# Kernel tuning notes

Measured on AMD Instinct MI355X. Metric: run time of the kernel, lower is better.

Reference implementation:

```python
import jax, jax.numpy as jnp
import numpy as np

N, M = 8192, 8192
N_POS, N_NEG = 2_000_000, 8_000_000


def setup_inputs() -> dict:
    key = jax.random.key(0)
    k1, k2, k3, k4, k5, k6, k7 = jax.random.split(key, 7)
    return {
        "drug_protein_reconstruct": jax.random.normal(k1, (N, M), dtype=jnp.float32),
        "drug_protein": jax.random.uniform(k2, (N, M), dtype=jnp.float32),
        "alpha": jax.random.uniform(k3, (1,), dtype=jnp.float32),
        "pos_x_index": jax.random.randint(k4, (N_POS,), 0, N, dtype=jnp.int64 if jax.config.jax_enable_x64 else jnp.int32),
        "pos_y_index": jax.random.randint(k5, (N_POS,), 0, M, dtype=jnp.int64 if jax.config.jax_enable_x64 else jnp.int32),
        "neg_x_index": jax.random.randint(k6, (N_NEG,), 0, N, dtype=jnp.int64 if jax.config.jax_enable_x64 else jnp.int32),
        "neg_y_index": jax.random.randint(k7, (N_NEG,), 0, M, dtype=jnp.int64 if jax.config.jax_enable_x64 else jnp.int32),
    }


def reference(drug_protein_reconstruct, drug_protein, alpha,
              pos_x_index, pos_y_index, neg_x_index, neg_y_index):
    # Fused gather -> subtract -> square -> sum (equivalent to dense MSE matrix
    # followed by fancy indexing, but without materializing the full loss_mat).
    a = alpha[0]
    pos_diff = (drug_protein_reconstruct[pos_x_index, pos_y_index]
                - drug_protein[pos_x_index, pos_y_index])
    neg_diff = (drug_protein_reconstruct[neg_x_index, neg_y_index]
                - drug_protein[neg_x_index, neg_y_index])
    pos_sum = jnp.sum(pos_diff * pos_diff)
    neg_sum = jnp.sum(neg_diff * neg_diff)
    return pos_sum * ((1.0 - a) * 0.5) + neg_sum * (a * 0.5)
```

## Files before the change

### kernel.cpp

```cpp
#include <hip/hip_runtime.h>

#define BLOCK 256
#define GRID  2048
#define NBUCK 256
#define PIPT  16
#define PCHUNK (BLOCK * PIPT)

typedef int v4i __attribute__((ext_vector_type(4)));

__device__ __forceinline__ void block_reduce_out(float pos_acc, float neg_acc,
                                                 const float* alpha, float* out) {
    const float a = alpha[0];
    float v = pos_acc * ((1.0f - a) * 0.5f) + neg_acc * (a * 0.5f);
    #pragma unroll
    for (int off = 32; off > 0; off >>= 1)
        v += __shfl_down(v, off, 64);
    __shared__ float sdata[BLOCK / 64];
    const int lane = threadIdx.x & 63;
    const int wave = threadIdx.x >> 6;
    if (lane == 0) sdata[wave] = v;
    __syncthreads();
    if (threadIdx.x == 0) {
        float s = 0.0f;
        #pragma unroll
        for (int w = 0; w < BLOCK / 64; ++w) s += sdata[w];
        if (s != 0.0f) atomicAdd(out, s);
    }
}

__global__ __launch_bounds__(BLOCK) void partition_kernel(
    const int* __restrict__ px, const int* __restrict__ py, int npos,
    const int* __restrict__ nx, const int* __restrict__ ny, int nneg,
    unsigned* __restrict__ items, unsigned* __restrict__ gcnt, int cap,
    const float* __restrict__ R, const float* __restrict__ D,
    const float* __restrict__ alpha, float* __restrict__ out)
{
    __shared__ unsigned s_cnt[NBUCK];
    __shared__ unsigned s_base[NBUCK];
    __shared__ unsigned s_cur[NBUCK];

    const int tid   = threadIdx.x;
    const int total = npos + nneg;
    const int nchunks = (total + PCHUNK - 1) / PCHUNK;

    float pos_acc = 0.0f, neg_acc = 0.0f;

    for (int c = blockIdx.x; c < nchunks; c += gridDim.x) {
        const int run = c * PCHUNK + tid * PIPT;
        const int nval = min(PIPT, max(0, total - run));

        unsigned it[PIPT];
        if (nval == PIPT && run + PIPT <= npos) {
            const v4i* x4 = (const v4i*)(px + run);
            const v4i* y4 = (const v4i*)(py + run);
            #pragma unroll
            for (int q = 0; q < PIPT / 4; ++q) {
                v4i xs = x4[q], ys = y4[q];
                it[q*4+0] = ((unsigned)xs.x << 13) | (unsigned)ys.x;
                it[q*4+1] = ((unsigned)xs.y << 13) | (unsigned)ys.y;
                it[q*4+2] = ((unsigned)xs.z << 13) | (unsigned)ys.z;
                it[q*4+3] = ((unsigned)xs.w << 13) | (unsigned)ys.w;
            }
        } else if (nval == PIPT && run >= npos && (((run - npos) & 3) == 0)) {
            const int j = run - npos;
            const v4i* x4 = (const v4i*)(nx + j);
            const v4i* y4 = (const v4i*)(ny + j);
            #pragma unroll
            for (int q = 0; q < PIPT / 4; ++q) {
                v4i xs = x4[q], ys = y4[q];
                it[q*4+0] = (((unsigned)xs.x << 13) | (unsigned)ys.x) | (1u << 26);
                it[q*4+1] = (((unsigned)xs.y << 13) | (unsigned)ys.y) | (1u << 26);
                it[q*4+2] = (((unsigned)xs.z << 13) | (unsigned)ys.z) | (1u << 26);
                it[q*4+3] = (((unsigned)xs.w << 13) | (unsigned)ys.w) | (1u << 26);
            }
        } else {
            for (int k = 0; k < PIPT; ++k) {
                const int gi = run + k;
                if (k < nval) {
                    if (gi < npos) it[k] = ((unsigned)px[gi] << 13) | (unsigned)py[gi];
                    else {
                        const int j = gi - npos;
                        it[k] = (((unsigned)nx[j] << 13) | (unsigned)ny[j]) | (1u << 26);
                    }
                } else it[k] = 0;
            }
        }

        s_cnt[tid] = 0;
        __syncthreads();
        #pragma unroll
        for (int k = 0; k < PIPT; ++k)
            if (k < nval) atomicAdd(&s_cnt[(it[k] >> 18) & 0xFF], 1u);
        __syncthreads();

        const unsigned cnt = s_cnt[tid];
        if (cnt) s_base[tid] = atomicAdd(&gcnt[tid], cnt);
        s_cur[tid] = 0;
        __syncthreads();

        #pragma unroll
        for (int k = 0; k < PIPT; ++k) {
            if (k < nval) {
                const unsigned b = (it[k] >> 18) & 0xFF;
                const unsigned p = atomicAdd(&s_cur[b], 1u);
                const unsigned gpos = s_base[b] + p;
                if (gpos < (unsigned)cap) {
                    items[(size_t)b * cap + gpos] = it[k];
                } else {
                    const unsigned o = it[k] & 0x3FFFFFFu;
                    const float d = R[o] - D[o];
                    if (it[k] >> 26) neg_acc += d * d; else pos_acc += d * d;
                }
            }
        }
        __syncthreads();
    }

    block_reduce_out(pos_acc, neg_acc, alpha, out);
}

__global__ __launch_bounds__(BLOCK) void gather_kernel(
    const float* __restrict__ R, const float* __restrict__ D,
    const float* __restrict__ alpha,
    const unsigned* __restrict__ items, const unsigned* __restrict__ gcnt,
    int cap, float* __restrict__ out)
{
    const int xcd = blockIdx.x & 7;
    const int g   = blockIdx.x >> 3;
    const unsigned team_stride = (GRID / 8) * BLOCK;

    float pos_acc = 0.0f, neg_acc = 0.0f;

    for (int bi = 0; bi < NBUCK / 8; ++bi) {
        const int b = bi * 8 + xcd;
        const unsigned n = min(gcnt[b], (unsigned)cap);
        const unsigned* ib = items + (size_t)b * cap;
        for (unsigned i = (unsigned)g * BLOCK + threadIdx.x; i < n; i += team_stride) {
            const unsigned it = ib[i];
            const unsigned o = it & 0x3FFFFFFu;
            const float d = R[o] - D[o];
            if (it >> 26) neg_acc += d * d; else pos_acc += d * d;
        }
    }

    block_reduce_out(pos_acc, neg_acc, alpha, out);
}

__global__ __launch_bounds__(BLOCK) void dti_direct_kernel(
    const float* __restrict__ R, const float* __restrict__ D,
    const float* __restrict__ alpha,
    const int* __restrict__ px, const int* __restrict__ py, int npos,
    const int* __restrict__ nx, const int* __restrict__ ny, int nneg,
    float* __restrict__ out)
{
    const int tid = blockIdx.x * BLOCK + threadIdx.x;
    const int stride = gridDim.x * BLOCK;
    float pos_acc = 0.0f, neg_acc = 0.0f;
    {
        const int n4 = npos >> 2;
        const v4i* px4 = (const v4i*)px;
        const v4i* py4 = (const v4i*)py;
        for (int i = tid; i < n4; i += stride) {
            v4i xs = px4[i], ys = py4[i];
            int o0 = (xs.x << 13) + ys.x, o1 = (xs.y << 13) + ys.y;
            int o2 = (xs.z << 13) + ys.z, o3 = (xs.w << 13) + ys.w;
            float d0 = R[o0]-D[o0], d1 = R[o1]-D[o1], d2 = R[o2]-D[o2], d3 = R[o3]-D[o3];
            pos_acc += d0*d0 + d1*d1 + d2*d2 + d3*d3;
        }
        for (int i = (n4 << 2) + tid; i < npos; i += stride) {
            int o = (px[i] << 13) + py[i];
            float d = R[o] - D[o];
            pos_acc += d * d;
        }
    }
    {
        const int n4 = nneg >> 2;
        const v4i* nx4 = (const v4i*)nx;
        const v4i* ny4 = (const v4i*)ny;
        for (int i = tid; i < n4; i += stride) {
            v4i xs = nx4[i], ys = ny4[i];
            int o0 = (xs.x << 13) + ys.x, o1 = (xs.y << 13) + ys.y;
            int o2 = (xs.z << 13) + ys.z, o3 = (xs.w << 13) + ys.w;
            float d0 = R[o0]-D[o0], d1 = R[o1]-D[o1], d2 = R[o2]-D[o2], d3 = R[o3]-D[o3];
            neg_acc += d0*d0 + d1*d1 + d2*d2 + d3*d3;
        }
        for (int i = (n4 << 2) + tid; i < nneg; i += stride) {
            int o = (nx[i] << 13) + ny[i];
            float d = R[o] - D[o];
            neg_acc += d * d;
        }
    }
    block_reduce_out(pos_acc, neg_acc, alpha, out);
}

extern "C" void kernel_launch(void* const* d_in, const int* in_sizes, int n_in,
                              void* d_out, int out_size, void* d_ws, size_t ws_size,
                              hipStream_t stream) {
    const float* R     = (const float*)d_in[0];
    const float* D     = (const float*)d_in[1];
    const float* alpha = (const float*)d_in[2];
    const int*   px    = (const int*)d_in[3];
    const int*   py    = (const int*)d_in[4];
    const int*   nx    = (const int*)d_in[5];
    const int*   ny    = (const int*)d_in[6];
    const int    npos  = in_sizes[3];
    const int    nneg  = in_sizes[5];
    const int    total = npos + nneg;

    float* out = (float*)d_out;
    hipMemsetAsync(out, 0, sizeof(float), stream);

    const int cap = total / NBUCK + total / (NBUCK * 4) + 1024;
    const size_t need = (size_t)NBUCK * cap * sizeof(unsigned) + NBUCK * sizeof(unsigned);

    if (d_ws != nullptr && ws_size >= need) {
        unsigned* items = (unsigned*)d_ws;
        unsigned* gcnt  = items + (size_t)NBUCK * cap;
        hipMemsetAsync(gcnt, 0, NBUCK * sizeof(unsigned), stream);
        partition_kernel<<<GRID, BLOCK, 0, stream>>>(
            px, py, npos, nx, ny, nneg, items, gcnt, cap, R, D, alpha, out);
        gather_kernel<<<GRID, BLOCK, 0, stream>>>(
            R, D, alpha, items, gcnt, cap, out);
    } else {
        dti_direct_kernel<<<GRID, BLOCK, 0, stream>>>(
            R, D, alpha, px, py, npos, nx, ny, nneg, out);
    }
}
```

Baseline: 708.1 us.

## Replace bucketed gather with dense per-element count histogram and streaming loss pass

Adds a path that scatters atomic increments into a byte-per-element count map, using 4-bit positive and 4-bit negative counts packed four elements per word. A second kernel then streams R and D as 16-byte vectors and weights each squared difference by its counts. This swaps random 4-byte gathers and the bucket partition for a mostly sequential sweep of both matrices. The cost is a 64MB memset, scattered global atomics and reading most of R and D. The 4-bit counters can overflow if one element is indexed more than 15 times.

```diff
diff --git a/kernel.cpp b/kernel.cpp
--- a/kernel.cpp
+++ b/kernel.cpp
@@ -6,7 +6,8 @@
 #define PIPT  16
 #define PCHUNK (BLOCK * PIPT)
 
-typedef int v4i __attribute__((ext_vector_type(4)));
+typedef int   v4i __attribute__((ext_vector_type(4)));
+typedef float v4f __attribute__((ext_vector_type(4)));
 
 __device__ __forceinline__ void block_reduce_out(float pos_acc, float neg_acc,
                                                  const float* alpha, float* out) {
@@ -28,6 +29,87 @@
     }
 }
 
+__global__ __launch_bounds__(BLOCK) void count_scatter_kernel(
+    const int* __restrict__ px, const int* __restrict__ py, int npos,
+    const int* __restrict__ nx, const int* __restrict__ ny, int nneg,
+    unsigned* __restrict__ cnt)
+{
+    const int tid    = blockIdx.x * BLOCK + threadIdx.x;
+    const int stride = GRID * BLOCK;
+
+    {
+        const int n4 = npos >> 2;
+        const v4i* x4 = (const v4i*)px;
+        const v4i* y4 = (const v4i*)py;
+        for (int i = tid; i < n4; i += stride) {
+            v4i xs = __builtin_nontemporal_load(&x4[i]);
+            v4i ys = __builtin_nontemporal_load(&y4[i]);
+            unsigned o0 = ((unsigned)xs.x << 13) + (unsigned)ys.x;
+            unsigned o1 = ((unsigned)xs.y << 13) + (unsigned)ys.y;
+            unsigned o2 = ((unsigned)xs.z << 13) + (unsigned)ys.z;
+            unsigned o3 = ((unsigned)xs.w << 13) + (unsigned)ys.w;
+            atomicAdd(&cnt[o0 >> 2], 1u << ((o0 & 3u) * 8u));
+            atomicAdd(&cnt[o1 >> 2], 1u << ((o1 & 3u) * 8u));
+            atomicAdd(&cnt[o2 >> 2], 1u << ((o2 & 3u) * 8u));
+            atomicAdd(&cnt[o3 >> 2], 1u << ((o3 & 3u) * 8u));
+        }
+        for (int i = (n4 << 2) + tid; i < npos; i += stride) {
+            unsigned o = ((unsigned)px[i] << 13) + (unsigned)py[i];
+            atomicAdd(&cnt[o >> 2], 1u << ((o & 3u) * 8u));
+        }
+    }
+    {
+        const int n4 = nneg >> 2;
+        const v4i* x4 = (const v4i*)nx;
+        const v4i* y4 = (const v4i*)ny;
+        for (int i = tid; i < n4; i += stride) {
+            v4i xs = __builtin_nontemporal_load(&x4[i]);
+            v4i ys = __builtin_nontemporal_load(&y4[i]);
+            unsigned o0 = ((unsigned)xs.x << 13) + (unsigned)ys.x;
+            unsigned o1 = ((unsigned)xs.y << 13) + (unsigned)ys.y;
+            unsigned o2 = ((unsigned)xs.z << 13) + (unsigned)ys.z;
+            unsigned o3 = ((unsigned)xs.w << 13) + (unsigned)ys.w;
+            atomicAdd(&cnt[o0 >> 2], 16u << ((o0 & 3u) * 8u));
+            atomicAdd(&cnt[o1 >> 2], 16u << ((o1 & 3u) * 8u));
+            atomicAdd(&cnt[o2 >> 2], 16u << ((o2 & 3u) * 8u));
+            atomicAdd(&cnt[o3 >> 2], 16u << ((o3 & 3u) * 8u));
+        }
+        for (int i = (n4 << 2) + tid; i < nneg; i += stride) {
+            unsigned o = ((unsigned)nx[i] << 13) + (unsigned)ny[i];
+            atomicAdd(&cnt[o >> 2], 16u << ((o & 3u) * 8u));
+        }
+    }
+}
+
+__global__ __launch_bounds__(BLOCK) void dense_loss_kernel(
+    const float* __restrict__ R, const float* __restrict__ D,
+    const float* __restrict__ alpha, const unsigned* __restrict__ cnt,
+    int nwords, float* __restrict__ out)
+{
+    const int tid    = blockIdx.x * BLOCK + threadIdx.x;
+    const int stride = GRID * BLOCK;
+    float pos_acc = 0.0f, neg_acc = 0.0f;
+
+    const v4f* R4 = (const v4f*)R;
+    const v4f* D4 = (const v4f*)D;
+    for (int w = tid; w < nwords; w += stride) {
+        const unsigned c = __builtin_nontemporal_load(&cnt[w]);
+        if (c) {
+            v4f r = __builtin_nontemporal_load(&R4[w]);
+            v4f d = __builtin_nontemporal_load(&D4[w]);
+            #pragma unroll
+            for (int j = 0; j < 4; ++j) {
+                const unsigned b = (c >> (j * 8)) & 0xFFu;
+                const float df = r[j] - d[j];
+                const float d2 = df * df;
+                pos_acc += d2 * (float)(b & 0xFu);
+                neg_acc += d2 * (float)(b >> 4);
+            }
+        }
+    }
+    block_reduce_out(pos_acc, neg_acc, alpha, out);
+}
+
 __global__ __launch_bounds__(BLOCK) void partition_kernel(
     const int* __restrict__ px, const int* __restrict__ py, int npos,
     const int* __restrict__ nx, const int* __restrict__ ny, int nneg,
@@ -93,8 +175,8 @@
             if (k < nval) atomicAdd(&s_cnt[(it[k] >> 18) & 0xFF], 1u);
         __syncthreads();
 
-        const unsigned cnt = s_cnt[tid];
-        if (cnt) s_base[tid] = atomicAdd(&gcnt[tid], cnt);
+        const unsigned cntv = s_cnt[tid];
+        if (cntv) s_base[tid] = atomicAdd(&gcnt[tid], cntv);
         s_cur[tid] = 0;
         __syncthreads();
 
@@ -205,15 +287,27 @@
     const int*   ny    = (const int*)d_in[6];
     const int    npos  = in_sizes[3];
     const int    nneg  = in_sizes[5];
+    const int    nelem = in_sizes[0];
     const int    total = npos + nneg;
 
     float* out = (float*)d_out;
     hipMemsetAsync(out, 0, sizeof(float), stream);
 
+    const size_t need_dense = (size_t)nelem;
+
+    if (d_ws != nullptr && ws_size >= need_dense) {
+        unsigned* cnt = (unsigned*)d_ws;
+        hipMemsetAsync(cnt, 0, need_dense, stream);
+        count_scatter_kernel<<<GRID, BLOCK, 0, stream>>>(
+            px, py, npos, nx, ny, nneg, cnt);
+        dense_loss_kernel<<<GRID, BLOCK, 0, stream>>>(
+            R, D, alpha, cnt, nelem >> 2, out);
+        return;
+    }
+
     const int cap = total / NBUCK + total / (NBUCK * 4) + 1024;
-    const size_t need = (size_t)NBUCK * cap * sizeof(unsigned) + NBUCK * sizeof(unsigned);
-
-    if (d_ws != nullptr && ws_size >= need) {
+    const size_t need_bucket = (size_t)NBUCK * cap * sizeof(unsigned) + NBUCK * sizeof(unsigned);
+    if (d_ws != nullptr && ws_size >= need_bucket) {
         unsigned* items = (unsigned*)d_ws;
         unsigned* gcnt  = items + (size_t)NBUCK * cap;
         hipMemsetAsync(gcnt, 0, NBUCK * sizeof(unsigned), stream);
@@ -221,8 +315,9 @@
             px, py, npos, nx, ny, nneg, items, gcnt, cap, R, D, alpha, out);
         gather_kernel<<<GRID, BLOCK, 0, stream>>>(
             R, D, alpha, items, gcnt, cap, out);
-    } else {
-        dti_direct_kernel<<<GRID, BLOCK, 0, stream>>>(
-            R, D, alpha, px, py, npos, nx, ny, nneg, out);
-    }
-}
+        return;
+    }
+
+    dti_direct_kernel<<<GRID, BLOCK, 0, stream>>>(
+        R, D, alpha, px, py, npos, nx, ny, nneg, out);
+}
```

Result: slower. 909.3 us (+28.4%).

## Stage partitioned items in LDS via block prefix scan for coalesced bucket stores

Applied to the files above, without the earlier changes.

The partition kernel now computes an exclusive prefix scan of per-bucket counts and scatters each chunk's items into a shared-memory buffer sorted by bucket. It then writes them out with consecutive threads handling consecutive slots, so global stores to each bucket become contiguous runs instead of scattered per-thread writes. Index loads and item stores use nontemporal hints, and cap is rounded to a multiple of 4. This adds 16KB of LDS per block and an extra barrier and pass, which may reduce occupancy.

```diff
diff --git a/kernel.cpp b/kernel.cpp
--- a/kernel.cpp
+++ b/kernel.cpp
@@ -36,8 +36,10 @@
     const float* __restrict__ alpha, float* __restrict__ out)
 {
     __shared__ unsigned s_cnt[NBUCK];
-    __shared__ unsigned s_base[NBUCK];
-    __shared__ unsigned s_cur[NBUCK];
+    __shared__ unsigned s_pos[NBUCK];
+    __shared__ unsigned s_gmo[NBUCK];
+    __shared__ unsigned s_wsum[BLOCK/64];
+    __shared__ unsigned s_items[PCHUNK];
 
     const int tid   = threadIdx.x;
     const int total = npos + nneg;
@@ -45,8 +47,8 @@
 
     float pos_acc = 0.0f, neg_acc = 0.0f;
 
-    for (int c = blockIdx.x; c < nchunks; c += gridDim.x) {
-        const int run = c * PCHUNK + tid * PIPT;
+    for (int c = blockIdx.x; c < nchunks; c += GRID) {
+        const int run  = c * PCHUNK + tid * PIPT;
         const int nval = min(PIPT, max(0, total - run));
 
         unsigned it[PIPT];
@@ -55,7 +57,8 @@
             const v4i* y4 = (const v4i*)(py + run);
             #pragma unroll
             for (int q = 0; q < PIPT / 4; ++q) {
-                v4i xs = x4[q], ys = y4[q];
+                v4i xs = __builtin_nontemporal_load(&x4[q]);
+                v4i ys = __builtin_nontemporal_load(&y4[q]);
                 it[q*4+0] = ((unsigned)xs.x << 13) | (unsigned)ys.x;
                 it[q*4+1] = ((unsigned)xs.y << 13) | (unsigned)ys.y;
                 it[q*4+2] = ((unsigned)xs.z << 13) | (unsigned)ys.z;
@@ -67,7 +70,8 @@
             const v4i* y4 = (const v4i*)(ny + j);
             #pragma unroll
             for (int q = 0; q < PIPT / 4; ++q) {
-                v4i xs = x4[q], ys = y4[q];
+                v4i xs = __builtin_nontemporal_load(&x4[q]);
+                v4i ys = __builtin_nontemporal_load(&y4[q]);
                 it[q*4+0] = (((unsigned)xs.x << 13) | (unsigned)ys.x) | (1u << 26);
                 it[q*4+1] = (((unsigned)xs.y << 13) | (unsigned)ys.y) | (1u << 26);
                 it[q*4+2] = (((unsigned)xs.z << 13) | (unsigned)ys.z) | (1u << 26);
@@ -93,23 +97,51 @@
             if (k < nval) atomicAdd(&s_cnt[(it[k] >> 18) & 0xFF], 1u);
         __syncthreads();
 
-        const unsigned cnt = s_cnt[tid];
-        if (cnt) s_base[tid] = atomicAdd(&gcnt[tid], cnt);
-        s_cur[tid] = 0;
+        const unsigned v = s_cnt[tid];
+        unsigned x = v;
+        #pragma unroll
+        for (int o = 1; o < 64; o <<= 1) {
+            unsigned t = __shfl_up(x, o, 64);
+            if ((tid & 63) >= o) x += t;
+        }
+        if ((tid & 63) == 63) s_wsum[tid >> 6] = x;
+        __syncthreads();
+        unsigned wpre = 0;
+        #pragma unroll
+        for (int w = 0; w < BLOCK / 64; ++w)
+            if (w < (tid >> 6)) wpre += s_wsum[w];
+        const unsigned excl = wpre + x - v;
+
+        unsigned gb = 0;
+        if (v) gb = atomicAdd(&gcnt[tid], v);
+        s_pos[tid] = excl;
+        s_gmo[tid] = gb - excl;
         __syncthreads();
 
         #pragma unroll
         for (int k = 0; k < PIPT; ++k) {
             if (k < nval) {
                 const unsigned b = (it[k] >> 18) & 0xFF;
-                const unsigned p = atomicAdd(&s_cur[b], 1u);
-                const unsigned gpos = s_base[b] + p;
+                const unsigned slot = atomicAdd(&s_pos[b], 1u);
+                s_items[slot] = it[k];
+            }
+        }
+        __syncthreads();
+
+        const unsigned chunk_total = (unsigned)min(total - c * PCHUNK, PCHUNK);
+        #pragma unroll
+        for (int k = 0; k < PIPT; ++k) {
+            const unsigned slot = (unsigned)(k * BLOCK) + tid;
+            if (slot < chunk_total) {
+                const unsigned itm = s_items[slot];
+                const unsigned b = (itm >> 18) & 0xFF;
+                const unsigned gpos = s_gmo[b] + slot;
                 if (gpos < (unsigned)cap) {
-                    items[(size_t)b * cap + gpos] = it[k];
+                    __builtin_nontemporal_store(itm, &items[(size_t)b * cap + gpos]);
                 } else {
-                    const unsigned o = it[k] & 0x3FFFFFFu;
+                    const unsigned o = itm & 0x3FFFFFFu;
                     const float d = R[o] - D[o];
-                    if (it[k] >> 26) neg_acc += d * d; else pos_acc += d * d;
+                    if (itm >> 26) neg_acc += d * d; else pos_acc += d * d;
                 }
             }
         }
@@ -210,7 +242,7 @@
     float* out = (float*)d_out;
     hipMemsetAsync(out, 0, sizeof(float), stream);
 
-    const int cap = total / NBUCK + total / (NBUCK * 4) + 1024;
+    const int cap = ((total / NBUCK + total / (NBUCK * 4) + 1024 + 3) & ~3);
     const size_t need = (size_t)NBUCK * cap * sizeof(unsigned) + NBUCK * sizeof(unsigned);
 
     if (d_ws != nullptr && ws_size >= need) {
```

Measured after the change: 716.3 us. About the same (+1.2%).
